# Performance work log

Measured on AMD Instinct MI355X. Metric: run time of the kernel, lower is better.

The kernel has to match this reference:

```python
import jax, jax.numpy as jnp
import numpy as np

D_MODEL = 1024
D_FF = 4096
NUM_HEADS = 16
D_HEAD = D_MODEL // NUM_HEADS
EPS = 1e-5


def setup_inputs() -> dict:
    key = jax.random.key(0)
    ks = jax.random.split(key, 16)
    s = 0.02
    return {
        "X": jax.random.normal(ks[0], (2, 2048, D_MODEL), dtype=jnp.float32),
        "W_qkv": jax.random.normal(ks[1], (D_MODEL, 3 * D_MODEL), dtype=jnp.float32) * s,
        "b_qkv": jax.random.normal(ks[2], (3 * D_MODEL,), dtype=jnp.float32) * s,
        "W_o": jax.random.normal(ks[3], (D_MODEL, D_MODEL), dtype=jnp.float32) * s,
        "b_o": jax.random.normal(ks[4], (D_MODEL,), dtype=jnp.float32) * s,
        "W_1": jax.random.normal(ks[5], (D_MODEL, D_FF), dtype=jnp.float32) * s,
        "b_1": jax.random.normal(ks[6], (D_FF,), dtype=jnp.float32) * s,
        "W_2": jax.random.normal(ks[7], (D_FF, D_MODEL), dtype=jnp.float32) * s,
        "b_2": jax.random.normal(ks[8], (D_MODEL,), dtype=jnp.float32) * s,
        "ln1_g": jnp.ones((D_MODEL,), dtype=jnp.float32),
        "ln1_b": jnp.zeros((D_MODEL,), dtype=jnp.float32),
        "ln2_g": jnp.ones((D_MODEL,), dtype=jnp.float32),
        "ln2_b": jnp.zeros((D_MODEL,), dtype=jnp.float32),
    }


def _layernorm(x, g, b):
    mu = jnp.mean(x, axis=-1, keepdims=True)
    var = jnp.mean(jnp.square(x - mu), axis=-1, keepdims=True)
    return (x - mu) * jax.lax.rsqrt(var + EPS) * g + b


def reference(X, W_qkv, b_qkv, W_o, b_o, W_1, b_1, W_2, b_2, ln1_g, ln1_b, ln2_g, ln2_b):
    B, T, D = X.shape
    qkv = X @ W_qkv + b_qkv                      # [B,T,3D]
    Q, K, V = jnp.split(qkv, 3, axis=-1)
    # [B,H,T,d]
    Q = Q.reshape(B, T, NUM_HEADS, D_HEAD).transpose(0, 2, 1, 3)
    K = K.reshape(B, T, NUM_HEADS, D_HEAD).transpose(0, 2, 1, 3)
    V = V.reshape(B, T, NUM_HEADS, D_HEAD).transpose(0, 2, 1, 3)
    scores = jnp.einsum('bhqd,bhkd->bhqk', Q, K) / np.float32(D_HEAD) ** 0.5
    causal = jnp.tril(jnp.ones((T, T), dtype=bool))
    scores = jnp.where(causal, scores, jnp.float32(-jnp.inf))
    A = jax.nn.softmax(scores, axis=-1)
    O = jnp.einsum('bhqk,bhkd->bhqd', A, V)
    O = O.transpose(0, 2, 1, 3).reshape(B, T, D)
    O = O @ W_o + b_o
    H_1 = _layernorm(X + O, ln1_g, ln1_b)
    H_2 = (jax.nn.gelu(H_1 @ W_1 + b_1, approximate=False)) @ W_2 + b_2
    return _layernorm(H_1 + H_2, ln2_g, ln2_b)
```

## Files before the change

kernel.cpp:

```cpp
#include <hip/hip_runtime.h>
#include <cmath>

typedef unsigned short u16;
typedef __bf16 bf16x8 __attribute__((ext_vector_type(8)));
typedef float f32x4 __attribute__((ext_vector_type(4)));

#define DEVI __device__ __forceinline__

DEVI float b2f(u16 u){ union{unsigned int i; float f;} v; v.i=(unsigned int)u<<16; return v.f; }
DEVI u16 f2b(float f){ union{unsigned int i; float f;} v; v.f=f;
    unsigned int r=(v.i+0x7FFFu+((v.i>>16)&1u))>>16; return (u16)r; }

DEVI void gload_lds16(const u16* g, u16* l){
    __builtin_amdgcn_global_load_lds((__attribute__((address_space(1))) void*)g,
                                     (__attribute__((address_space(3))) void*)l,
                                     16, 0, 0);
}

__global__ __launch_bounds__(256)
void cvt_bf16(const float* __restrict__ in, u16* __restrict__ out)
{
    const int i = (blockIdx.x * 256 + threadIdx.x) * 4;
    float4 v = *(const float4*)&in[i];
    ushort4 o;
    o.x = f2b(v.x); o.y = f2b(v.y); o.z = f2b(v.z); o.w = f2b(v.w);
    *(ushort4*)&out[i] = o;
}

__global__ __launch_bounds__(256)
void cvt_transpose(const float* __restrict__ in, u16* __restrict__ out, int R, int C)
{
    __shared__ __align__(16) u16 tile[64*72];
    const int rb = blockIdx.x*64, cb = blockIdx.y*64;
    const int t = threadIdx.x;
    const int r = t >> 3, c0 = (t & 7) * 8;
    #pragma unroll
    for (int rr = 0; rr < 2; rr++) {
        const int row = r + rr*32;
        float4 a = *(const float4*)&in[(long)(rb + row)*C + cb + c0];
        float4 b = *(const float4*)&in[(long)(rb + row)*C + cb + c0 + 4];
        u16* tp = &tile[row*72 + c0];
        tp[0]=f2b(a.x); tp[1]=f2b(a.y); tp[2]=f2b(a.z); tp[3]=f2b(a.w);
        tp[4]=f2b(b.x); tp[5]=f2b(b.y); tp[6]=f2b(b.z); tp[7]=f2b(b.w);
    }
    __syncthreads();
    #pragma unroll
    for (int rr = 0; rr < 2; rr++) {
        const int cr = r + rr*32;
        u16 tmp[8];
        #pragma unroll
        for (int j = 0; j < 8; j++) tmp[j] = tile[(c0 + j)*72 + cr];
        *(uint4*)&out[(long)(cb + cr)*R + rb + c0] = *(uint4*)tmp;
    }
}

template<int EPI, int BM>
__global__ __launch_bounds__(256)
void gemm_bt(const u16* __restrict__ A, const u16* __restrict__ Bt,
             const float* __restrict__ bias, const u16* __restrict__ Res,
             u16* __restrict__ C, u16* __restrict__ C2, int M, int N, int K)
{
    constexpr int RM = BM / 32;
    constexpr int NA = (BM / 16) * 2 / 4;
    __shared__ __align__(16) u16 As[BM*64];
    __shared__ __align__(16) u16 Bs[128*64];
    const int tid  = threadIdx.x;
    const int wave = tid >> 6, lane = tid & 63;
    const int tm = blockIdx.x * BM, tn = blockIdx.y * 128;

    const int rs = lane >> 2, cs = (lane & 3) * 8;
    const u16* gA[NA]; u16* lA[NA];
    #pragma unroll
    for (int i = 0; i < NA; i++) {
        const int c = wave + i*4;
        const int p = c / (BM/16), rb = c % (BM/16);
        gA[i] = A + (long)(tm + rb*16 + rs)*K + p*32 + cs;
        lA[i] = As + p*(BM*32) + rb*512;
    }
    const u16* gB[4]; u16* lB[4];
    #pragma unroll
    for (int i = 0; i < 4; i++) {
        const int c = wave + i*4;
        const int p = c >> 3, rb = c & 7;
        gB[i] = Bt + (long)(tn + rb*16 + rs)*K + p*32 + cs;
        lB[i] = Bs + p*(128*32) + rb*512;
    }

    const int wm = (wave >> 1) * (BM/2), wn = (wave & 1) * 64;
    const int fr = lane & 15, fq = lane >> 4;

    f32x4 acc[RM][4] = {};
    for (int k0 = 0; k0 < K; k0 += 64) {
        __syncthreads();
        #pragma unroll
        for (int i = 0; i < NA; i++) gload_lds16(gA[i] + k0, lA[i]);
        #pragma unroll
        for (int i = 0; i < 4; i++)  gload_lds16(gB[i] + k0, lB[i]);
        __syncthreads();
        #pragma unroll
        for (int p = 0; p < 2; p++) {
            bf16x8 af[RM], bfr[4];
            #pragma unroll
            for (int i = 0; i < RM; i++)
                af[i]  = *(const bf16x8*)&As[p*(BM*32) + (wm + i*16 + fr)*32 + fq*8];
            #pragma unroll
            for (int j = 0; j < 4; j++)
                bfr[j] = *(const bf16x8*)&Bs[p*(128*32) + (wn + j*16 + fr)*32 + fq*8];
            #pragma unroll
            for (int i = 0; i < RM; i++)
                #pragma unroll
                for (int j = 0; j < 4; j++)
                    acc[i][j] = __builtin_amdgcn_mfma_f32_16x16x32_bf16(af[i], bfr[j], acc[i][j], 0, 0, 0);
        }
    }

    #pragma unroll
    for (int i = 0; i < RM; i++) {
        const int row = tm + wm + i*16 + fq*4;
        #pragma unroll
        for (int j = 0; j < 4; j++) {
            const int col = tn + wn + j*16 + fr;
            const float bv = bias[col];
            if (EPI == 3 && col >= 2048) {
                const int hh = (col - 2048) >> 6, dd = (col - 2048) & 63;
                const int batch = row >> 11, tok = row & 2047;
                u16 pk[4];
                #pragma unroll
                for (int r = 0; r < 4; r++) pk[r] = f2b(acc[i][j][r] + bv);
                *(uint2*)&C2[((long)(batch*16 + hh)*64 + dd)*2048 + tok] = *(uint2*)pk;
            } else {
                const int cw = (EPI == 3) ? 2048 : N;
                #pragma unroll
                for (int r = 0; r < 4; r++) {
                    float v = acc[i][j][r] + bv;
                    const long idx = (long)(row + r)*cw + col;
                    if (EPI == 1) v += b2f(Res[idx]);
                    if (EPI == 2) {
                        const float u = v + 0.044715f*v*v*v;
                        const float t = exp2f(u * 2.302208f);
                        v = v * t * __builtin_amdgcn_rcpf(t + 1.f);
                    }
                    C[idx] = f2b(v);
                }
            }
        }
    }
}

__global__ __launch_bounds__(512)
void attn_kernel(const u16* __restrict__ QK, const u16* __restrict__ VT,
                 u16* __restrict__ O)
{
    constexpr float CS = 0.18033688011112042f;
    __shared__ __align__(16) u16 smem[40960];

    const int tid = threadIdx.x, wave = tid >> 6, lane = tid & 63;
    const int grp = wave >> 2, wg = wave & 3;
    const int pair = blockIdx.x, h = blockIdx.y, b = blockIdx.z;
    const int fr = lane & 15, fq = lane >> 4;
    const long qkbase = (long)b*2048*2048;
    const long vtbase = (long)(b*16 + h)*64*2048;
    const int rs = lane >> 2, cs2 = (lane & 3) * 8;
    const int sw = (fr & 7) * 8;
    const int KsBase = grp*8192;
    const int VsBase = 16384 + grp*8192;
    u16* pw = &smem[32768 + wave*1024];

    #define ISSUE(bf, k0)                                                      \
        _Pragma("unroll")                                                      \
        for (int i = 0; i < 2; i++) {                                          \
            const int c = wg + i*4;                                            \
            const int kp = c >> 2, krb = c & 3;                                \
            gload_lds16(QK + qkbase + (long)((k0) + krb*16 + rs)*2048          \
                           + 1024 + h*64 + kp*32 + cs2,                        \
                        &smem[KsBase + (bf)*4096 + kp*2048 + krb*512]);        \
            const int vp = c & 1, vrb = c >> 1;                                \
            gload_lds16(VT + vtbase + (long)(vrb*16 + rs)*2048                 \
                           + (k0) + vp*32 + cs2,                               \
                        &smem[VsBase + (bf)*4096 + vp*2048 + vrb*512]);        \
        }

    #pragma unroll 1
    for (int which = 0; which < 2; which++) {
        const int qt = which ? pair : (31 - pair);

        bf16x8 bq[2];
        #pragma unroll
        for (int ks = 0; ks < 2; ks++)
            bq[ks] = *(const bf16x8*)&QK[qkbase + (long)(qt*64 + wg*16 + fr)*2048
                                         + h*64 + ks*32 + fq*8];

        const int q_glob = qt*64 + wg*16 + fr;
        const int q_wmin = qt*64 + wg*16;
        f32x4 o[4] = {};
        float m_i = -1e30f, l_i = 0.f;
        const int nkt = qt + 1;
        const int nit = (nkt + 1) >> 1;
        const int myn = (nkt + 1 - grp) >> 1;

        if (which) __syncthreads();
        if (grp < nkt) { ISSUE(0, grp*64) }

        for (int it = 0; it < nit; it++) {
            const int kt = 2*it + grp;
            const int k0 = kt * 64;
            const int cur = it & 1;
            __syncthreads();
            if (kt + 2 < nkt) { ISSUE(cur ^ 1, k0 + 128) }

            if (it < myn) {
                f32x4 st[4];
                #pragma unroll
                for (int mt = 0; mt < 4; mt++) st[mt] = (f32x4){0.f,0.f,0.f,0.f};
                #pragma unroll
                for (int mt = 0; mt < 4; mt++)
                    #pragma unroll
                    for (int ks = 0; ks < 2; ks++) {
                        bf16x8 ak = *(const bf16x8*)&smem[KsBase + cur*4096 + ks*2048 + (mt*16 + fr)*32 + fq*8];
                        st[mt] = __builtin_amdgcn_mfma_f32_16x16x32_bf16(ak, bq[ks], st[mt], 0, 0, 0);
                    }

                float mx = -1e30f;
                if (k0 + 63 > q_wmin) {
                    #pragma unroll
                    for (int mt = 0; mt < 4; mt++)
                        #pragma unroll
                        for (int r = 0; r < 4; r++) {
                            const int key = k0 + mt*16 + fq*4 + r;
                            float v = st[mt][r];
                            if (key > q_glob) v = -1e30f;
                            st[mt][r] = v;
                            mx = fmaxf(mx, v);
                        }
                } else {
                    #pragma unroll
                    for (int mt = 0; mt < 4; mt++)
                        #pragma unroll
                        for (int r = 0; r < 4; r++) mx = fmaxf(mx, st[mt][r]);
                }
                mx = fmaxf(mx, __shfl_xor(mx, 16, 64));
                mx = fmaxf(mx, __shfl_xor(mx, 32, 64));

                if (mx > m_i + 44.357f) {
                    const float alpha = exp2f((m_i - mx) * CS);
                    #pragma unroll
                    for (int dt = 0; dt < 4; dt++)
                        #pragma unroll
                        for (int r = 0; r < 4; r++) o[dt][r] *= alpha;
                    l_i *= alpha;
                    m_i = mx;
                }
                const float nms = -m_i * CS;
                float ps = 0.f;
                #pragma unroll
                for (int mt = 0; mt < 4; mt++)
                    #pragma unroll
                    for (int r = 0; r < 4; r++) {
                        const float p = exp2f(fmaf(st[mt][r], CS, nms));
                        st[mt][r] = p; ps += p;
                    }
                ps += __shfl_xor(ps, 16, 64);
                ps += __shfl_xor(ps, 32, 64);
                l_i += ps;

                #pragma unroll
                for (int mt = 0; mt < 4; mt++)
                    #pragma unroll
                    for (int d = 0; d < 2; d++) {
                        unsigned pk;
                        asm("v_cvt_pk_bf16_f32 %0, %1, %2"
                            : "=v"(pk) : "v"(st[mt][2*d]), "v"(st[mt][2*d+1]));
                        *(unsigned*)&pw[fr*64 + ((mt*16 + fq*4 + 2*d) ^ sw)] = pk;
                    }
                __asm__ volatile("" ::: "memory");
                bf16x8 bp[2];
                #pragma unroll
                for (int kk = 0; kk < 2; kk++)
                    bp[kk] = *(const bf16x8*)&pw[fr*64 + ((kk*32 + fq*8) ^ sw)];
                #pragma unroll
                for (int dt = 0; dt < 4; dt++)
                    #pragma unroll
                    for (int kk = 0; kk < 2; kk++) {
                        bf16x8 av = *(const bf16x8*)&smem[VsBase + cur*4096 + kk*2048 + (dt*16 + fr)*32 + fq*8];
                        o[dt] = __builtin_amdgcn_mfma_f32_16x16x32_bf16(av, bp[kk], o[dt], 0, 0, 0);
                    }
                __asm__ volatile("" ::: "memory");
            }
        }

        __syncthreads();
        float* MB = (float*)&smem[8192];
        float* ML = (float*)&smem[24576];
        if (grp == 1) {
            #pragma unroll
            for (int dt = 0; dt < 4; dt++)
                *(f32x4*)&MB[(wg*64 + lane)*16 + dt*4] = o[dt];
            if (fq == 0) {
                ML[(wg*16 + fr)*2]     = m_i;
                ML[(wg*16 + fr)*2 + 1] = l_i;
            }
        }
        __syncthreads();
        if (grp == 0) {
            const float m1 = ML[(wg*16 + fr)*2];
            const float l1 = ML[(wg*16 + fr)*2 + 1];
            const float m  = fmaxf(m_i, m1);
            const float e0 = exp2f((m_i - m) * CS);
            const float e1 = exp2f((m1  - m) * CS);
            const float rl = __builtin_amdgcn_rcpf(l_i*e0 + l1*e1);
            const long orow = (long)b*2048 + qt*64 + wg*16 + fr;
            #pragma unroll
            for (int dt = 0; dt < 4; dt++) {
                f32x4 o1 = *(const f32x4*)&MB[(wg*64 + lane)*16 + dt*4];
                u16 pk[4];
                #pragma unroll
                for (int r = 0; r < 4; r++)
                    pk[r] = f2b((o[dt][r]*e0 + o1[r]*e1) * rl);
                *(uint2*)&O[orow*1024 + h*64 + dt*16 + fq*4] = *(uint2*)pk;
            }
        }
    }
    #undef ISSUE
}

template<int OUTF32>
__global__ __launch_bounds__(256)
void ln_kernel(const u16* __restrict__ X, const float* __restrict__ G,
               const float* __restrict__ B, void* __restrict__ Yv)
{
    __shared__ float red[8];
    const int tid = threadIdx.x;
    const long row = blockIdx.x;
    const u16* x = X + row*1024;
    ushort4 u = *(const ushort4*)&x[tid*4];
    const float v0 = b2f(u.x), v1 = b2f(u.y), v2 = b2f(u.z), v3 = b2f(u.w);
    float s = v0+v1+v2+v3;
    float q = v0*v0+v1*v1+v2*v2+v3*v3;
    #pragma unroll
    for (int off = 32; off >= 1; off >>= 1) {
        s += __shfl_xor(s, off, 64);
        q += __shfl_xor(q, off, 64);
    }
    const int wv = tid >> 6;
    if ((tid & 63) == 0) { red[wv*2] = s; red[wv*2+1] = q; }
    __syncthreads();
    s = red[0]+red[2]+red[4]+red[6];
    q = red[1]+red[3]+red[5]+red[7];
    const float mu = s * (1.f/1024.f);
    const float rstd = rsqrtf(fmaxf(q*(1.f/1024.f) - mu*mu, 0.f) + 1e-5f);
    float4 g4 = *(const float4*)&G[tid*4];
    float4 b4 = *(const float4*)&B[tid*4];
    const float y0 = (v0-mu)*rstd*g4.x + b4.x;
    const float y1 = (v1-mu)*rstd*g4.y + b4.y;
    const float y2 = (v2-mu)*rstd*g4.z + b4.z;
    const float y3 = (v3-mu)*rstd*g4.w + b4.w;
    if (OUTF32) {
        float4 o = make_float4(y0, y1, y2, y3);
        *(float4*)&((float*)Yv)[row*1024 + tid*4] = o;
    } else {
        ushort4 o;
        o.x = f2b(y0); o.y = f2b(y1); o.z = f2b(y2); o.w = f2b(y3);
        *(ushort4*)&((u16*)Yv)[row*1024 + tid*4] = o;
    }
}

extern "C" void kernel_launch(void* const* d_in, const int* in_sizes, int n_in,
                              void* d_out, int out_size, void* d_ws, size_t ws_size,
                              hipStream_t stream)
{
    const float* X    = (const float*)d_in[0];
    const float* Wqkv = (const float*)d_in[1];
    const float* bqkv = (const float*)d_in[2];
    const float* Wo   = (const float*)d_in[3];
    const float* bo   = (const float*)d_in[4];
    const float* W1   = (const float*)d_in[5];
    const float* b1   = (const float*)d_in[6];
    const float* W2   = (const float*)d_in[7];
    const float* b2   = (const float*)d_in[8];
    const float* g1   = (const float*)d_in[9];
    const float* be1  = (const float*)d_in[10];
    const float* g2   = (const float*)d_in[11];
    const float* be2  = (const float*)d_in[12];
    float* out = (float*)d_out;

    char* ws = (char*)d_ws;
    u16* Xbf   = (u16*)(ws + 0);
    u16* WqkvT = (u16*)(ws + 8388608);
    u16* WoT   = (u16*)(ws + 14680064);
    u16* QK    = (u16*)(ws + 16777216);
    u16* VT    = (u16*)(ws + 33554432);
    u16* AO    = (u16*)(ws + 41943040);
    u16* S1    = (u16*)(ws + 16777216);
    u16* H1    = (u16*)(ws + 0);
    u16* Gbuf  = (u16*)(ws + 8388608);
    u16* S2    = (u16*)(ws + 41943040);
    u16* W1T   = (u16*)d_out;
    u16* W2T   = (u16*)d_out + 4194304;

    cvt_bf16<<<4096, 256, 0, stream>>>(X, Xbf);
    cvt_transpose<<<dim3(16, 48), 256, 0, stream>>>(Wqkv, WqkvT, 1024, 3072);
    cvt_transpose<<<dim3(16, 16), 256, 0, stream>>>(Wo,   WoT,   1024, 1024);
    cvt_transpose<<<dim3(16, 64), 256, 0, stream>>>(W1,   W1T,   1024, 4096);
    cvt_transpose<<<dim3(64, 16), 256, 0, stream>>>(W2,   W2T,   4096, 1024);

    gemm_bt<3,128><<<dim3(32, 24), 256, 0, stream>>>(Xbf, WqkvT, bqkv, nullptr, QK, VT, 4096, 3072, 1024);
    attn_kernel<<<dim3(16, 16, 2), 512, 0, stream>>>(QK, VT, AO);
    gemm_bt<1,64><<<dim3(64, 8), 256, 0, stream>>>(AO, WoT, bo, Xbf, S1, nullptr, 4096, 1024, 1024);
    ln_kernel<0><<<4096, 256, 0, stream>>>(S1, g1, be1, H1);
    gemm_bt<2,128><<<dim3(32, 32), 256, 0, stream>>>(H1, W1T, b1, nullptr, Gbuf, nullptr, 4096, 4096, 1024);
    gemm_bt<1,64><<<dim3(64, 8), 256, 0, stream>>>(Gbuf, W2T, b2, H1, S2, nullptr, 4096, 1024, 4096);
    ln_kernel<1><<<4096, 256, 0, stream>>>(S2, g2, be2, out);
}
```

Measured before the change: 364.1 us.

## Split-K the output-projection and FFN-down GEMMs with atomic fp32 partials fused into layernorm

The N=1024 GEMMs (attention output projection and FFN down-projection) now run as split-K over two halves of K with fp32 atomicAdd into zeroed partial buffers, doubling grid size to improve CU occupancy. Bias and residual addition move into a fused layernorm kernel that reads the fp32 partials directly. This adds memset launches, atomic traffic, and fp32 intermediate reads/writes in exchange for more parallelism, and also reshuffles workspace aliasing (W1T/W2T positions, partial buffer placement in the output buffer).

New measurement: 396.2 us. +8.8%, slower.

```diff
diff --git a/kernel.cpp b/kernel.cpp
--- a/kernel.cpp
+++ b/kernel.cpp
@@ -147,6 +147,84 @@
     }
 }
 
+template<int BM>
+__global__ __launch_bounds__(256)
+void gemm_bt_split(const u16* __restrict__ A, const u16* __restrict__ Bt,
+                   float* __restrict__ Pa, float* __restrict__ Pb,
+                   int M, int N, int Khalf, int ldk)
+{
+    constexpr int RM = BM / 32;
+    constexpr int NA = (BM / 16) * 2 / 4;
+    __shared__ __align__(16) u16 As[BM*64];
+    __shared__ __align__(16) u16 Bs[128*64];
+    const int tid  = threadIdx.x;
+    const int wave = tid >> 6, lane = tid & 63;
+    const int tm = blockIdx.x * BM, tn = blockIdx.y * 128;
+    const int koff = blockIdx.z * Khalf;
+
+    const int rs = lane >> 2, cs = (lane & 3) * 8;
+    const u16* gA[NA]; u16* lA[NA];
+    #pragma unroll
+    for (int i = 0; i < NA; i++) {
+        const int c = wave + i*4;
+        const int p = c / (BM/16), rb = c % (BM/16);
+        gA[i] = A + (long)(tm + rb*16 + rs)*ldk + koff + p*32 + cs;
+        lA[i] = As + p*(BM*32) + rb*512;
+    }
+    const u16* gB[4]; u16* lB[4];
+    #pragma unroll
+    for (int i = 0; i < 4; i++) {
+        const int c = wave + i*4;
+        const int p = c >> 3, rb = c & 7;
+        gB[i] = Bt + (long)(tn + rb*16 + rs)*ldk + koff + p*32 + cs;
+        lB[i] = Bs + p*(128*32) + rb*512;
+    }
+
+    const int wm = (wave >> 1) * (BM/2), wn = (wave & 1) * 64;
+    const int fr = lane & 15, fq = lane >> 4;
+
+    f32x4 acc[RM][4] = {};
+    for (int k0 = 0; k0 < Khalf; k0 += 64) {
+        __syncthreads();
+        #pragma unroll
+        for (int i = 0; i < NA; i++) gload_lds16(gA[i] + k0, lA[i]);
+        #pragma unroll
+        for (int i = 0; i < 4; i++)  gload_lds16(gB[i] + k0, lB[i]);
+        __syncthreads();
+        #pragma unroll
+        for (int p = 0; p < 2; p++) {
+            bf16x8 af[RM], bfr[4];
+            #pragma unroll
+            for (int i = 0; i < RM; i++)
+                af[i]  = *(const bf16x8*)&As[p*(BM*32) + (wm + i*16 + fr)*32 + fq*8];
+            #pragma unroll
+            for (int j = 0; j < 4; j++)
+                bfr[j] = *(const bf16x8*)&Bs[p*(128*32) + (wn + j*16 + fr)*32 + fq*8];
+            #pragma unroll
+            for (int i = 0; i < RM; i++)
+                #pragma unroll
+                for (int j = 0; j < 4; j++)
+                    acc[i][j] = __builtin_amdgcn_mfma_f32_16x16x32_bf16(af[i], bfr[j], acc[i][j], 0, 0, 0);
+        }
+    }
+
+    #pragma unroll
+    for (int i = 0; i < RM; i++) {
+        const int row = tm + wm + i*16 + fq*4;
+        #pragma unroll
+        for (int j = 0; j < 4; j++) {
+            const int col = tn + wn + j*16 + fr;
+            #pragma unroll
+            for (int r = 0; r < 4; r++) {
+                const int row4 = row + r;
+                float* P = (row4 < 2048) ? (Pa + (long)row4*N + col)
+                                         : (Pb + (long)(row4 - 2048)*N + col);
+                atomicAdd(P, acc[i][j][r]);
+            }
+        }
+    }
+}
+
 __global__ __launch_bounds__(512)
 void attn_kernel(const u16* __restrict__ QK, const u16* __restrict__ VT,
                  u16* __restrict__ O)
@@ -325,15 +403,22 @@
 
 template<int OUTF32>
 __global__ __launch_bounds__(256)
-void ln_kernel(const u16* __restrict__ X, const float* __restrict__ G,
-               const float* __restrict__ B, void* __restrict__ Yv)
+void ln_fused(const float* __restrict__ Pa, const float* __restrict__ Pb,
+              const float* __restrict__ bias, const u16* __restrict__ Res,
+              const float* __restrict__ G, const float* __restrict__ B,
+              void* __restrict__ Yv)
 {
     __shared__ float red[8];
     const int tid = threadIdx.x;
     const long row = blockIdx.x;
-    const u16* x = X + row*1024;
-    ushort4 u = *(const ushort4*)&x[tid*4];
-    const float v0 = b2f(u.x), v1 = b2f(u.y), v2 = b2f(u.z), v3 = b2f(u.w);
+    const float* p = (row < 2048) ? (Pa + row*1024) : (Pb + (row - 2048)*1024);
+    float4 pv = *(const float4*)&p[tid*4];
+    float4 bb = *(const float4*)&bias[tid*4];
+    ushort4 rr = *(const ushort4*)&Res[row*1024 + tid*4];
+    const float v0 = pv.x + bb.x + b2f(rr.x);
+    const float v1 = pv.y + bb.y + b2f(rr.y);
+    const float v2 = pv.z + bb.z + b2f(rr.z);
+    const float v3 = pv.w + bb.w + b2f(rr.w);
     float s = v0+v1+v2+v3;
     float q = v0*v0+v1*v1+v2*v2+v3*v3;
     #pragma unroll
@@ -390,12 +475,13 @@
     u16* QK    = (u16*)(ws + 16777216);
     u16* VT    = (u16*)(ws + 33554432);
     u16* AO    = (u16*)(ws + 41943040);
-    u16* S1    = (u16*)(ws + 16777216);
+    float* P1  = (float*)(ws + 25165824);
     u16* H1    = (u16*)(ws + 0);
     u16* Gbuf  = (u16*)(ws + 8388608);
-    u16* S2    = (u16*)(ws + 41943040);
-    u16* W1T   = (u16*)d_out;
-    u16* W2T   = (u16*)d_out + 4194304;
+    float* Pa2 = (float*)(ws + 41943040);
+    u16* W2T   = (u16*)d_out;
+    u16* W1T   = (u16*)d_out + 4194304;
+    float* Pb2 = (float*)d_out + 2097152;
 
     cvt_bf16<<<4096, 256, 0, stream>>>(X, Xbf);
     cvt_transpose<<<dim3(16, 48), 256, 0, stream>>>(Wqkv, WqkvT, 1024, 3072);
@@ -405,9 +491,15 @@
 
     gemm_bt<3,128><<<dim3(32, 24), 256, 0, stream>>>(Xbf, WqkvT, bqkv, nullptr, QK, VT, 4096, 3072, 1024);
     attn_kernel<<<dim3(16, 16, 2), 512, 0, stream>>>(QK, VT, AO);
-    gemm_bt<1,64><<<dim3(64, 8), 256, 0, stream>>>(AO, WoT, bo, Xbf, S1, nullptr, 4096, 1024, 1024);
-    ln_kernel<0><<<4096, 256, 0, stream>>>(S1, g1, be1, H1);
+
+    hipMemsetAsync(P1, 0, 16777216, stream);
+    gemm_bt_split<64><<<dim3(64, 8, 2), 256, 0, stream>>>(AO, WoT, P1, P1 + 2048*1024, 4096, 1024, 512, 1024);
+    ln_fused<0><<<4096, 256, 0, stream>>>(P1, P1 + 2048*1024, bo, Xbf, g1, be1, H1);
+
     gemm_bt<2,128><<<dim3(32, 32), 256, 0, stream>>>(H1, W1T, b1, nullptr, Gbuf, nullptr, 4096, 4096, 1024);
-    gemm_bt<1,64><<<dim3(64, 8), 256, 0, stream>>>(Gbuf, W2T, b2, H1, S2, nullptr, 4096, 1024, 4096);
-    ln_kernel<1><<<4096, 256, 0, stream>>>(S2, g2, be2, out);
-}
+
+    hipMemsetAsync(Pa2, 0, 8388608, stream);
+    hipMemsetAsync(Pb2, 0, 8388608, stream);
+    gemm_bt_split<64><<<dim3(64, 8, 2), 256, 0, stream>>>(Gbuf, W2T, Pa2, Pb2, 4096, 1024, 2048, 4096);
+    ln_fused<1><<<4096, 256, 0, stream>>>(Pa2, Pb2, b2, H1, g2, be2, out);
+}
```

## Double-buffer LDS tiles in BM=64 GEMMs to overlap loads with MFMA

Applied to the files above, without the earlier changes.

Adds a DBUF template flag to gemm_bt that allocates two LDS stages for the A and B tiles. The next K-tile's global_load_lds is issued right after the barrier, before the MFMA work on the current tile, so each iteration needs one barrier instead of two. It is enabled only for the BM=64 output-projection and W2 GEMMs, which have fewer rows per block to hide latency. The cost is double the LDS footprint (48KB per block), which may limit how many blocks fit on a CU.

Measured after the change: 347.1 us. 1.05x faster.

```diff
diff --git a/kernel.cpp b/kernel.cpp
--- a/kernel.cpp
+++ b/kernel.cpp
@@ -54,7 +54,7 @@
     }
 }
 
-template<int EPI, int BM>
+template<int EPI, int BM, int DBUF>
 __global__ __launch_bounds__(256)
 void gemm_bt(const u16* __restrict__ A, const u16* __restrict__ Bt,
              const float* __restrict__ bias, const u16* __restrict__ Res,
@@ -62,8 +62,9 @@
 {
     constexpr int RM = BM / 32;
     constexpr int NA = (BM / 16) * 2 / 4;
-    __shared__ __align__(16) u16 As[BM*64];
-    __shared__ __align__(16) u16 Bs[128*64];
+    constexpr int ASZ = BM*64, BSZ = 128*64;
+    __shared__ __align__(16) u16 As[(DBUF ? 2 : 1)*ASZ];
+    __shared__ __align__(16) u16 Bs[(DBUF ? 2 : 1)*BSZ];
     const int tid  = threadIdx.x;
     const int wave = tid >> 6, lane = tid & 63;
     const int tm = blockIdx.x * BM, tn = blockIdx.y * 128;
@@ -90,27 +91,64 @@
     const int fr = lane & 15, fq = lane >> 4;
 
     f32x4 acc[RM][4] = {};
-    for (int k0 = 0; k0 < K; k0 += 64) {
-        __syncthreads();
+
+    if constexpr (DBUF) {
+        const int nk = K >> 6;
         #pragma unroll
-        for (int i = 0; i < NA; i++) gload_lds16(gA[i] + k0, lA[i]);
+        for (int i = 0; i < NA; i++) gload_lds16(gA[i], lA[i]);
         #pragma unroll
-        for (int i = 0; i < 4; i++)  gload_lds16(gB[i] + k0, lB[i]);
-        __syncthreads();
-        #pragma unroll
-        for (int p = 0; p < 2; p++) {
-            bf16x8 af[RM], bfr[4];
-            #pragma unroll
-            for (int i = 0; i < RM; i++)
-                af[i]  = *(const bf16x8*)&As[p*(BM*32) + (wm + i*16 + fr)*32 + fq*8];
-            #pragma unroll
-            for (int j = 0; j < 4; j++)
-                bfr[j] = *(const bf16x8*)&Bs[p*(128*32) + (wn + j*16 + fr)*32 + fq*8];
-            #pragma unroll
-            for (int i = 0; i < RM; i++)
+        for (int i = 0; i < 4; i++)  gload_lds16(gB[i], lB[i]);
+        for (int t = 0; t < nk; t++) {
+            __syncthreads();
+            if (t + 1 < nk) {
+                const int nb = (t + 1) & 1;
+                const int k0 = (t + 1) << 6;
+                #pragma unroll
+                for (int i = 0; i < NA; i++) gload_lds16(gA[i] + k0, lA[i] + nb*ASZ);
+                #pragma unroll
+                for (int i = 0; i < 4; i++)  gload_lds16(gB[i] + k0, lB[i] + nb*BSZ);
+            }
+            const u16* Ab = As + (t & 1)*ASZ;
+            const u16* Bb = Bs + (t & 1)*BSZ;
+            #pragma unroll
+            for (int p = 0; p < 2; p++) {
+                bf16x8 af[RM], bfr[4];
+                #pragma unroll
+                for (int i = 0; i < RM; i++)
+                    af[i]  = *(const bf16x8*)&Ab[p*(BM*32) + (wm + i*16 + fr)*32 + fq*8];
                 #pragma unroll
                 for (int j = 0; j < 4; j++)
-                    acc[i][j] = __builtin_amdgcn_mfma_f32_16x16x32_bf16(af[i], bfr[j], acc[i][j], 0, 0, 0);
+                    bfr[j] = *(const bf16x8*)&Bb[p*(128*32) + (wn + j*16 + fr)*32 + fq*8];
+                #pragma unroll
+                for (int i = 0; i < RM; i++)
+                    #pragma unroll
+                    for (int j = 0; j < 4; j++)
+                        acc[i][j] = __builtin_amdgcn_mfma_f32_16x16x32_bf16(af[i], bfr[j], acc[i][j], 0, 0, 0);
+            }
+        }
+    } else {
+        for (int k0 = 0; k0 < K; k0 += 64) {
+            __syncthreads();
+            #pragma unroll
+            for (int i = 0; i < NA; i++) gload_lds16(gA[i] + k0, lA[i]);
+            #pragma unroll
+            for (int i = 0; i < 4; i++)  gload_lds16(gB[i] + k0, lB[i]);
+            __syncthreads();
+            #pragma unroll
+            for (int p = 0; p < 2; p++) {
+                bf16x8 af[RM], bfr[4];
+                #pragma unroll
+                for (int i = 0; i < RM; i++)
+                    af[i]  = *(const bf16x8*)&As[p*(BM*32) + (wm + i*16 + fr)*32 + fq*8];
+                #pragma unroll
+                for (int j = 0; j < 4; j++)
+                    bfr[j] = *(const bf16x8*)&Bs[p*(128*32) + (wn + j*16 + fr)*32 + fq*8];
+                #pragma unroll
+                for (int i = 0; i < RM; i++)
+                    #pragma unroll
+                    for (int j = 0; j < 4; j++)
+                        acc[i][j] = __builtin_amdgcn_mfma_f32_16x16x32_bf16(af[i], bfr[j], acc[i][j], 0, 0, 0);
+            }
         }
     }
 
@@ -403,11 +441,11 @@
     cvt_transpose<<<dim3(16, 64), 256, 0, stream>>>(W1,   W1T,   1024, 4096);
     cvt_transpose<<<dim3(64, 16), 256, 0, stream>>>(W2,   W2T,   4096, 1024);
 
-    gemm_bt<3,128><<<dim3(32, 24), 256, 0, stream>>>(Xbf, WqkvT, bqkv, nullptr, QK, VT, 4096, 3072, 1024);
+    gemm_bt<3,128,0><<<dim3(32, 24), 256, 0, stream>>>(Xbf, WqkvT, bqkv, nullptr, QK, VT, 4096, 3072, 1024);
     attn_kernel<<<dim3(16, 16, 2), 512, 0, stream>>>(QK, VT, AO);
-    gemm_bt<1,64><<<dim3(64, 8), 256, 0, stream>>>(AO, WoT, bo, Xbf, S1, nullptr, 4096, 1024, 1024);
+    gemm_bt<1,64,1><<<dim3(64, 8), 256, 0, stream>>>(AO, WoT, bo, Xbf, S1, nullptr, 4096, 1024, 1024);
     ln_kernel<0><<<4096, 256, 0, stream>>>(S1, g1, be1, H1);
-    gemm_bt<2,128><<<dim3(32, 32), 256, 0, stream>>>(H1, W1T, b1, nullptr, Gbuf, nullptr, 4096, 4096, 1024);
-    gemm_bt<1,64><<<dim3(64, 8), 256, 0, stream>>>(Gbuf, W2T, b2, H1, S2, nullptr, 4096, 1024, 4096);
+    gemm_bt<2,128,0><<<dim3(32, 32), 256, 0, stream>>>(H1, W1T, b1, nullptr, Gbuf, nullptr, 4096, 4096, 1024);
+    gemm_bt<1,64,1><<<dim3(64, 8), 256, 0, stream>>>(Gbuf, W2T, b2, H1, S2, nullptr, 4096, 1024, 4096);
     ln_kernel<1><<<4096, 256, 0, stream>>>(S2, g2, be2, out);
 }
```
